# Kernel tuning notes

Measured on AMD Instinct MI355X. Metric: run time of the kernel, lower is better.

## Reference

```python
import jax, jax.numpy as jnp
import numpy as np

N = 50000      # nodes
E = 800000     # edges (before self-loops)
F_IN = 128     # num_features
H = 4          # heads
C = 64         # hidden_channels
HC = H * C     # 256
NEG_SLOPE = 0.2


def setup_inputs() -> dict:
    key = jax.random.key(0)
    ks = jax.random.split(key, 20)
    x = jax.random.normal(ks[0], (N, F_IN), dtype=jnp.float32)
    edge_index = jax.random.randint(ks[1], (2, E), 0, N, dtype=jnp.int32)
    s = 0.05
    inp = {"x": x, "edge_index": edge_index}
    dims_in = [F_IN, HC, HC, HC]
    for l in range(4):
        kW, ka, kb = jax.random.split(ks[2 + l], 3)
        inp[f"W{l+1}"] = jax.random.normal(kW, (dims_in[l], HC), dtype=jnp.float32) * s
        inp[f"a_src{l+1}"] = jax.random.normal(ka, (H, C), dtype=jnp.float32) * s
        inp[f"a_dst{l+1}"] = jax.random.normal(kb, (H, C), dtype=jnp.float32) * s
        inp[f"b{l+1}"] = jnp.zeros((HC,), dtype=jnp.float32)
    return inp


def gat_conv(x, src, dst, W, a_src, a_dst, b):
    # x: [N, F_in] -> h: [N, H, C]
    h = (x @ W).reshape(N, H, C)
    es = jnp.sum(h * a_src, axis=-1)  # [N, H] per-node source logits
    ed = jnp.sum(h * a_dst, axis=-1)  # [N, H]
    e = jax.nn.leaky_relu(es[src] + ed[dst], NEG_SLOPE)  # [Etot, H]
    m = jax.ops.segment_max(e, dst, num_segments=N)      # per-dst max
    m = jnp.where(jnp.isfinite(m), m, 0.0)
    ex = jnp.exp(e - m[dst])
    denom = jax.ops.segment_sum(ex, dst, num_segments=N)
    alpha = ex / (denom[dst] + 1e-16)                     # edge softmax
    out = jax.ops.segment_sum(alpha[:, :, None] * h[src], dst, num_segments=N)
    return out.reshape(N, HC) + b


def reference(x, edge_index,
              W1, a_src1, a_dst1, b1,
              W2, a_src2, a_dst2, b2,
              W3, a_src3, a_dst3, b3,
              W4, a_src4, a_dst4, b4):
    loop = jnp.arange(N, dtype=edge_index.dtype)
    src = jnp.concatenate([edge_index[0], loop])  # add self-loops (PyG default)
    dst = jnp.concatenate([edge_index[1], loop])
    x1 = jax.nn.relu(gat_conv(x, src, dst, W1, a_src1, a_dst1, b1))
    x2 = jax.nn.relu(gat_conv(x1, src, dst, W2, a_src2, a_dst2, b2))
    x3 = jax.nn.relu(gat_conv(x2 + x1, src, dst, W3, a_src3, a_dst3, b3))
    x4 = jax.nn.relu(gat_conv(x2 + x3, src, dst, W4, a_src4, a_dst4, b4))
    # NOTE: source code calls conv4 again (not conv5) -- reproduced faithfully
    x5 = gat_conv(x4 + x3, src, dst, W4, a_src4, a_dst4, b4)
    return x5
```

## Files before the change

### kernel.cpp

```cpp
#include <hip/hip_runtime.h>
#include <hip/hip_bf16.h>

#define N_NODES 50000
#define E_EDGES 800000
#define ETOT (E_EDGES + N_NODES)
#define HC 256
#define NHEAD 4
#define CHAN 64
#define NEG 0.2f
#define NBLK ((N_NODES + 1023) / 1024)

typedef _Float16 half8 __attribute__((ext_vector_type(8)));
typedef _Float16 half4v __attribute__((ext_vector_type(4)));
typedef float float4v __attribute__((ext_vector_type(4)));


__global__ __launch_bounds__(256) void count_rank_kernel(const int* __restrict__ ei,
                                                         int* __restrict__ counts,
                                                         int* __restrict__ rank) {
    int base = blockIdx.x * 1024 + threadIdx.x;
    int dst[4];
    bool val[4];
    #pragma unroll
    for (int r = 0; r < 4; ++r) {
        int i = base + r * 256;
        val[r] = (i < ETOT);
        dst[r] = 0;
        if (val[r]) dst[r] = (i < E_EDGES) ? ei[E_EDGES + i] : (i - E_EDGES);
    }
    int rk[4];
    #pragma unroll
    for (int r = 0; r < 4; ++r)
        if (val[r]) rk[r] = atomicAdd(&counts[dst[r]], 1);
    #pragma unroll
    for (int r = 0; r < 4; ++r)
        if (val[r]) rank[base + r * 256] = rk[r];
}

__global__ __launch_bounds__(256) void blocksum_kernel(const int* __restrict__ counts,
                                                       int* __restrict__ blocksums) {
    __shared__ int s[4];
    int b = blockIdx.x, tid = threadIdx.x;
    int base = b * 1024;
    int sum = 0;
    #pragma unroll
    for (int r = 0; r < 4; ++r) {
        int idx = base + r * 256 + tid;
        sum += (idx < N_NODES) ? counts[idx] : 0;
    }
    #pragma unroll
    for (int m = 1; m < 64; m <<= 1) sum += __shfl_xor(sum, m, 64);
    if ((tid & 63) == 0) s[tid >> 6] = sum;
    __syncthreads();
    if (tid == 0) blocksums[b] = s[0] + s[1] + s[2] + s[3];
}

__global__ __launch_bounds__(64) void blockscan_kernel(int* __restrict__ blocksums) {
    int tid = threadIdx.x;
    int v = (tid < NBLK) ? blocksums[tid] : 0;
    #pragma unroll
    for (int off = 1; off < 64; off <<= 1) {
        int t = __shfl_up(v, off, 64);
        if (tid >= off) v += t;
    }
    if (tid < NBLK) blocksums[tid] = v;
}

__global__ __launch_bounds__(1024) void scatter_scan_kernel(const int* __restrict__ counts,
                                                            const int* __restrict__ blocksums,
                                                            int* __restrict__ offsets) {
    __shared__ int s[1024];
    int b = blockIdx.x, tid = threadIdx.x;
    int idx = b * 1024 + tid;
    int v = (idx < N_NODES) ? counts[idx] : 0;
    s[tid] = v;
    __syncthreads();
    for (int off = 1; off < 1024; off <<= 1) {
        int t = (tid >= off) ? s[tid - off] : 0;
        __syncthreads();
        s[tid] += t;
        __syncthreads();
    }
    int excl = s[tid] - v + (b > 0 ? blocksums[b - 1] : 0);
    if (idx < N_NODES) offsets[idx] = excl;
    if (idx == N_NODES - 1) offsets[N_NODES] = excl + v;
}

__global__ __launch_bounds__(256) void fill_kernel(const int* __restrict__ ei,
                                                   const int* __restrict__ rank,
                                                   const int* __restrict__ offsets,
                                                   int2* __restrict__ csr) {
    int base = blockIdx.x * 1024 + threadIdx.x;
    #pragma unroll
    for (int r = 0; r < 4; ++r) {
        int i = base + r * 256;
        if (i >= ETOT) continue;
        int src, dst;
        if (i < E_EDGES) { src = ei[i]; dst = ei[E_EDGES + i]; }
        else             { src = i - E_EDGES; dst = src; }
        int pos = offsets[dst] + rank[i];
        csr[pos] = make_int2(src, dst);
    }
}


__global__ __launch_bounds__(256) void wsplit_all_kernel(
        const float* __restrict__ W0, const float* __restrict__ W1,
        const float* __restrict__ W2, const float* __restrict__ W3,
        _Float16* __restrict__ Th0, _Float16* __restrict__ Tl0,
        _Float16* __restrict__ Th1, _Float16* __restrict__ Tl1,
        _Float16* __restrict__ Th2, _Float16* __restrict__ Tl2,
        _Float16* __restrict__ Th3, _Float16* __restrict__ Tl3) {
    int id = blockIdx.x * 256 + threadIdx.x;
    const float* W; _Float16 *Th, *Tl; int K;
    if (id < 32768)       { W = W0; Th = Th0; Tl = Tl0; K = 128; }
    else if (id < 98304)  { W = W1; Th = Th1; Tl = Tl1; K = 256; id -= 32768; }
    else if (id < 163840) { W = W2; Th = Th2; Tl = Tl2; K = 256; id -= 98304; }
    else if (id < 229376) { W = W3; Th = Th3; Tl = Tl3; K = 256; id -= 163840; }
    else return;
    int n = id & 255, k = id >> 8;
    float w = W[(size_t)k * 256 + n];
    _Float16 h = (_Float16)w;
    _Float16 l = (_Float16)(w - (float)h);
    Th[(size_t)n * K + k] = h;
    Tl[(size_t)n * K + k] = l;
}

__global__ void xsplit_kernel(const float* __restrict__ x, _Float16* __restrict__ xh,
                              _Float16* __restrict__ xl, int total) {
    int id = blockIdx.x * 256 + threadIdx.x;
    if (id >= total) return;
    float v = x[id];
    _Float16 h = (_Float16)v;
    xh[id] = h;
    xl[id] = (_Float16)(v - (float)h);
}


__global__ __launch_bounds__(256) void edge_alpha_kernel(
        const float* __restrict__ es, const float* __restrict__ ed,
        const int2* __restrict__ csr, _Float16* __restrict__ ex) {
    int e = blockIdx.x * 256 + threadIdx.x;
    if (e >= ETOT) return;
    int2 sd = csr[e];
    float4 esv = *(const float4*)(es + (size_t)sd.x * 4);
    float4 edv = *(const float4*)(ed + (size_t)sd.y * 4);
    float4 v;
    v.x = esv.x + edv.x; v.y = esv.y + edv.y;
    v.z = esv.z + edv.z; v.w = esv.w + edv.w;
    v.x = (v.x > 0.f) ? v.x : NEG * v.x;
    v.y = (v.y > 0.f) ? v.y : NEG * v.y;
    v.z = (v.z > 0.f) ? v.z : NEG * v.z;
    v.w = (v.w > 0.f) ? v.w : NEG * v.w;
    half4v o = {(_Float16)__expf(v.x), (_Float16)__expf(v.y),
                (_Float16)__expf(v.z), (_Float16)__expf(v.w)};
    *(half4v*)(ex + (size_t)e * 4) = o;
}


template<int K, bool HASLO>
struct SmemLayout {
    _Float16 Ah[64][K + 8];
    _Float16 Al[HASLO ? 64 : 1][HASLO ? (K + 8) : 8];
    _Float16 Bh[256][40];
    _Float16 Bl[256][40];
};
template<int K, bool HASLO>
union SmemU {
    SmemLayout<K, HASLO> t;
    _Float16 out[64][264];
};

template<int K, bool HASLO, bool HAS2>
__global__ __launch_bounds__(256) void gemm_mfma_kernel(
        const _Float16* __restrict__ A1h, const _Float16* __restrict__ A1l,
        const _Float16* __restrict__ A2h,
        const _Float16* __restrict__ Wth, const _Float16* __restrict__ Wtl,
        const float* __restrict__ a_src, const float* __restrict__ a_dst,
        _Float16* __restrict__ H16, float* __restrict__ es, float* __restrict__ ed,
        int M) {
    constexpr int NC  = K / 32;
    constexpr int CPR = K / 8;
    __shared__ SmemU<K, HASLO> u;
    auto& Ah = u.t.Ah;
    auto& Al = u.t.Al;
    auto& Bh = u.t.Bh;
    auto& Bl = u.t.Bl;

    int tid = threadIdx.x;
    int m0 = blockIdx.x * 64;
    int w = tid >> 6, lane = tid & 63;
    int rn = w * 64;
    int fr = lane & 15;
    int q  = lane >> 4;
    int fk = q * 8;

    int wr = tid >> 2;
    int wk = (tid & 3) * 8;

    half8 a1c[NC], a2c[HAS2 ? NC : 1], alc[HASLO ? NC : 1];
    #pragma unroll
    for (int c = 0; c < NC; ++c) {
        int idx = c * 256 + tid;
        int row = idx / CPR, col = (idx % CPR) * 8;
        int grow = m0 + row;
        a1c[c] = (half8)(_Float16)0;
        if (grow < M) a1c[c] = *(const half8*)(A1h + (size_t)grow * K + col);
        if constexpr (HAS2) {
            a2c[c] = (half8)(_Float16)0;
            if (grow < M) a2c[c] = *(const half8*)(A2h + (size_t)grow * K + col);
        }
        if constexpr (HASLO) {
            alc[c] = (half8)(_Float16)0;
            if (grow < M) alc[c] = *(const half8*)(A1l + (size_t)grow * K + col);
        }
    }
    half8 pbh[4], pbl[4];
    auto loadB = [&](int k0) {
        #pragma unroll
        for (int g = 0; g < 4; ++g) {
            int r = g * 64 + wr;
            pbh[g] = *(const half8*)(Wth + (size_t)r * K + k0 + wk);
            pbl[g] = *(const half8*)(Wtl + (size_t)r * K + k0 + wk);
        }
    };
    loadB(0);

    #pragma unroll
    for (int c = 0; c < NC; ++c) {
        int idx = c * 256 + tid;
        int row = idx / CPR, col = (idx % CPR) * 8;
        half8 v = a1c[c];
        if constexpr (HAS2) v = v + a2c[c];
        *(half8*)&Ah[row][col] = v;
        if constexpr (HASLO) *(half8*)&Al[row][col] = alc[c];
    }

    float4v acc[4][4];
    #pragma unroll
    for (int i = 0; i < 4; ++i)
        #pragma unroll
        for (int j = 0; j < 4; ++j)
            acc[i][j] = (float4v){0.f, 0.f, 0.f, 0.f};

    __syncthreads();

    for (int kk = 0; kk < K / 32; ++kk) {
        int k0 = kk * 32;
        #pragma unroll
        for (int g = 0; g < 4; ++g) {
            int r = g * 64 + wr;
            *(half8*)&Bh[r][wk] = pbh[g];
            *(half8*)&Bl[r][wk] = pbl[g];
        }
        __syncthreads();
        if (kk + 1 < K / 32) loadB(k0 + 32);
        half8 afh[4], bfh[4], bfl[4];
        #pragma unroll
        for (int t = 0; t < 4; ++t) {
            afh[t] = *(const half8*)&Ah[t * 16 + fr][k0 + fk];
            bfh[t] = *(const half8*)&Bh[rn + t * 16 + fr][fk];
            bfl[t] = *(const half8*)&Bl[rn + t * 16 + fr][fk];
        }
        if constexpr (HASLO) {
            half8 afl[4];
            #pragma unroll
            for (int t = 0; t < 4; ++t) afl[t] = *(const half8*)&Al[t * 16 + fr][k0 + fk];
            #pragma unroll
            for (int tm = 0; tm < 4; ++tm)
                #pragma unroll
                for (int tn = 0; tn < 4; ++tn)
                    acc[tm][tn] = __builtin_amdgcn_mfma_f32_16x16x32_f16(
                        afl[tm], bfh[tn], acc[tm][tn], 0, 0, 0);
        }
        #pragma unroll
        for (int tm = 0; tm < 4; ++tm)
            #pragma unroll
            for (int tn = 0; tn < 4; ++tn) {
                float4v c = acc[tm][tn];
                c = __builtin_amdgcn_mfma_f32_16x16x32_f16(afh[tm], bfl[tn], c, 0, 0, 0);
                c = __builtin_amdgcn_mfma_f32_16x16x32_f16(afh[tm], bfh[tn], c, 0, 0, 0);
                acc[tm][tn] = c;
            }
        __syncthreads();
    }

    float asv[4], adv[4];
    #pragma unroll
    for (int tn = 0; tn < 4; ++tn) {
        asv[tn] = a_src[w * CHAN + tn * 16 + fr];
        adv[tn] = a_dst[w * CHAN + tn * 16 + fr];
    }
    #pragma unroll
    for (int tm = 0; tm < 4; ++tm) {
        #pragma unroll
        for (int i = 0; i < 4; ++i) {
            int r = tm * 16 + q * 4 + i;
            float ps = 0.f, pd = 0.f;
            #pragma unroll
            for (int tn = 0; tn < 4; ++tn) {
                float hv = acc[tm][tn][i];
                ps += hv * asv[tn];
                pd += hv * adv[tn];
                u.out[r][rn + tn * 16 + fr] = (_Float16)hv;
            }
            #pragma unroll
            for (int msk = 1; msk < 16; msk <<= 1) {
                ps += __shfl_xor(ps, msk, 64);
                pd += __shfl_xor(pd, msk, 64);
            }
            int row = m0 + r;
            if (fr == 0 && row < M) {
                es[row * NHEAD + w] = ps;
                ed[row * NHEAD + w] = pd;
            }
        }
    }
    __syncthreads();

    #pragma unroll
    for (int k = 0; k < 8; ++k) {
        int c = k * 256 + tid;
        int r = c >> 5, cc = c & 31;
        if (m0 + r < M) {
            half8 v = *(const half8*)(&u.out[r][0] + cc * 8);
            *(half8*)(H16 + (size_t)(m0 + r) * HC + cc * 8) = v;
        }
    }
}


__global__ __launch_bounds__(256) void gat_aggregate_kernel(
        const _Float16* __restrict__ H16, const _Float16* __restrict__ ex,
        const int* __restrict__ offsets, const int2* __restrict__ csr,
        const float* __restrict__ bias, _Float16* __restrict__ out16,
        float* __restrict__ out32, int do_relu, int node_base) {
    __shared__ float ex_lds[4][256];
    __shared__ int   src_lds[4][64];
    int tid = threadIdx.x;
    int w = tid >> 6, lane = tid & 63;
    int n = node_base + blockIdx.x * 4 + w;
    int off = offsets[n];
    int deg = offsets[n + 1] - off;

    if (deg <= 64) {
        int sreg = n;
        half4v exh = (half4v)(_Float16)0;
        if (lane < deg) {
            sreg = csr[off + lane].x;
            exh = *(const half4v*)(ex + (size_t)(off + lane) * 4);
        }
        float4 ex4 = make_float4((float)exh[0], (float)exh[1], (float)exh[2], (float)exh[3]);
        src_lds[w][lane] = sreg;
        *(float4*)&ex_lds[w][lane * 4] = ex4;

        int hl = lane & 31, side = lane >> 5;
        int hd = hl >> 3;
        float av[8] = {0.f, 0.f, 0.f, 0.f, 0.f, 0.f, 0.f, 0.f};
        int degr = (deg + 7) & ~7;
        #pragma unroll 2
        for (int j0 = 0; j0 < degr; j0 += 8) {
            int j = j0 + side;
            int s0 = src_lds[w][j];
            int s1 = src_lds[w][j + 2];
            int s2 = src_lds[w][j + 4];
            int s3 = src_lds[w][j + 6];
            float w0 = ex_lds[w][j * 4 + hd];
            float w1 = ex_lds[w][(j + 2) * 4 + hd];
            float w2 = ex_lds[w][(j + 4) * 4 + hd];
            float w3 = ex_lds[w][(j + 6) * 4 + hd];
            half8 h0 = *(const half8*)(H16 + (size_t)s0 * HC + hl * 8);
            half8 h1 = *(const half8*)(H16 + (size_t)s1 * HC + hl * 8);
            half8 h2 = *(const half8*)(H16 + (size_t)s2 * HC + hl * 8);
            half8 h3 = *(const half8*)(H16 + (size_t)s3 * HC + hl * 8);
            #pragma unroll
            for (int c = 0; c < 8; ++c) {
                av[c] += w0 * (float)h0[c];
                av[c] += w1 * (float)h1[c];
                av[c] += w2 * (float)h2[c];
                av[c] += w3 * (float)h3[c];
            }
        }

        float4 l4 = ex4;
        #pragma unroll
        for (int msk = 1; msk < 64; msk <<= 1) {
            l4.x += __shfl_xor(l4.x, msk, 64);
            l4.y += __shfl_xor(l4.y, msk, 64);
            l4.z += __shfl_xor(l4.z, msk, 64);
            l4.w += __shfl_xor(l4.w, msk, 64);
        }
        #pragma unroll
        for (int c = 0; c < 8; ++c) av[c] += __shfl_xor(av[c], 32, 64);
        if (side == 0) {
            float denom = (hd == 0) ? l4.x : (hd == 1) ? l4.y : (hd == 2) ? l4.z : l4.w;
            float scale = 1.f / (denom + 1e-16f);
            float4 b0 = *(const float4*)(bias + hl * 8);
            float4 b1 = *(const float4*)(bias + hl * 8 + 4);
            float o[8] = {av[0] * scale + b0.x, av[1] * scale + b0.y,
                          av[2] * scale + b0.z, av[3] * scale + b0.w,
                          av[4] * scale + b1.x, av[5] * scale + b1.y,
                          av[6] * scale + b1.z, av[7] * scale + b1.w};
            if (do_relu)
                #pragma unroll
                for (int c = 0; c < 8; ++c) o[c] = fmaxf(o[c], 0.f);
            if (out16) {
                half8 ov = {(_Float16)o[0], (_Float16)o[1], (_Float16)o[2], (_Float16)o[3],
                            (_Float16)o[4], (_Float16)o[5], (_Float16)o[6], (_Float16)o[7]};
                *(half8*)(out16 + (size_t)n * HC + hl * 8) = ov;
            } else {
                *(float4*)(out32 + (size_t)n * HC + hl * 8) =
                    make_float4(o[0], o[1], o[2], o[3]);
                *(float4*)(out32 + (size_t)n * HC + hl * 8 + 4) =
                    make_float4(o[4], o[5], o[6], o[7]);
            }
        }
        return;
    }

    int head = lane >> 4;
    float4 acc0 = make_float4(0.f, 0.f, 0.f, 0.f);
    float den = 0.f;
    for (int j = 0; j < deg; ++j) {
        int s = csr[off + j].x;
        float exv = (float)ex[(size_t)(off + j) * 4 + head];
        den += exv;
        half4v h0 = *(const half4v*)(H16 + (size_t)s * HC + lane * 4);
        acc0.x += exv * (float)h0[0]; acc0.y += exv * (float)h0[1];
        acc0.z += exv * (float)h0[2]; acc0.w += exv * (float)h0[3];
    }
    float scale = 1.f / (den + 1e-16f);
    float4 b4 = *(const float4*)(bias + lane * 4);
    float o[4] = {acc0.x * scale + b4.x, acc0.y * scale + b4.y,
                  acc0.z * scale + b4.z, acc0.w * scale + b4.w};
    if (do_relu)
        #pragma unroll
        for (int c = 0; c < 4; ++c) o[c] = fmaxf(o[c], 0.f);
    if (out16) {
        half4v ov = {(_Float16)o[0], (_Float16)o[1], (_Float16)o[2], (_Float16)o[3]};
        *(half4v*)(out16 + (size_t)n * HC + lane * 4) = ov;
    } else {
        *(float4*)(out32 + (size_t)n * HC + lane * 4) = make_float4(o[0], o[1], o[2], o[3]);
    }
}


extern "C" void kernel_launch(void* const* d_in, const int* in_sizes, int n_in,
                              void* d_out, int out_size, void* d_ws, size_t ws_size,
                              hipStream_t stream) {
    const float* x  = (const float*)d_in[0];
    const int*   ei = (const int*)d_in[1];
    const float *W[5], *Asrc[5], *Adst[5], *Bs[5];
    for (int l = 0; l < 4; ++l) {
        W[l]    = (const float*)d_in[2 + l * 4];
        Asrc[l] = (const float*)d_in[3 + l * 4];
        Adst[l] = (const float*)d_in[4 + l * 4];
        Bs[l]   = (const float*)d_in[5 + l * 4];
    }
    W[4] = W[3]; Asrc[4] = Asrc[3]; Adst[4] = Adst[3]; Bs[4] = Bs[3];

    char* ws = (char*)d_ws;
    size_t off = 0;
    auto alloc = [&](size_t bytes) -> void* {
        void* p = ws + off;
        off += (bytes + 255) & ~(size_t)255;
        return p;
    };
    _Float16* h16  = (_Float16*)alloc((size_t)N_NODES * HC * 2);
    _Float16* xa   = (_Float16*)alloc((size_t)N_NODES * HC * 2);
    _Float16* xb   = (_Float16*)alloc((size_t)N_NODES * HC * 2);
    _Float16* xc   = (_Float16*)alloc((size_t)N_NODES * HC * 2);
    _Float16* xd   = (_Float16*)alloc((size_t)N_NODES * HC * 2);
    _Float16* xh   = (_Float16*)alloc((size_t)N_NODES * 128 * 2);
    _Float16* xl   = (_Float16*)alloc((size_t)N_NODES * 128 * 2);
    float* es      = (float*)alloc((size_t)N_NODES * 4 * 4);
    float* ed      = (float*)alloc((size_t)N_NODES * 4 * 4);
    _Float16* exbuf = (_Float16*)alloc((size_t)ETOT * 4 * 2);
    int*   counts  = (int*)alloc((size_t)N_NODES * 4);
    int*   offsets = (int*)alloc((size_t)(N_NODES + 1) * 4);
    int*   rank    = (int*)alloc((size_t)ETOT * 4);
    int2*  csr     = (int2*)alloc((size_t)ETOT * 8);
    int*   blocksums = (int*)alloc((size_t)NBLK * 4);
    _Float16 *Wth[5], *Wtl[5];
    int Ks[4] = {128, 256, 256, 256};
    for (int l = 0; l < 4; ++l) {
        Wth[l] = (_Float16*)alloc((size_t)256 * Ks[l] * 2);
        Wtl[l] = (_Float16*)alloc((size_t)256 * Ks[l] * 2);
    }
    Wth[4] = Wth[3]; Wtl[4] = Wtl[3];

    hipMemsetAsync(counts, 0, (size_t)N_NODES * 4, stream);
    count_rank_kernel<<<(ETOT + 1023) / 1024, 256, 0, stream>>>(ei, counts, rank);
    blocksum_kernel<<<NBLK, 256, 0, stream>>>(counts, blocksums);
    blockscan_kernel<<<1, 64, 0, stream>>>(blocksums);
    scatter_scan_kernel<<<NBLK, 1024, 0, stream>>>(counts, blocksums, offsets);
    fill_kernel<<<(ETOT + 1023) / 1024, 256, 0, stream>>>(ei, rank, offsets, csr);
    wsplit_all_kernel<<<(229376 + 255) / 256, 256, 0, stream>>>(
        W[0], W[1], W[2], W[3],
        Wth[0], Wtl[0], Wth[1], Wtl[1], Wth[2], Wtl[2], Wth[3], Wtl[3]);
    xsplit_kernel<<<(N_NODES * 128 + 255) / 256, 256, 0, stream>>>(x, xh, xl, N_NODES * 128);

    int gemm_grid = (N_NODES + 63) / 64;
    auto agg = [&](int l, _Float16* o16, float* o32, int relu) {
        edge_alpha_kernel<<<(ETOT + 255) / 256, 256, 0, stream>>>(
            es, ed, csr, exbuf);
        gat_aggregate_kernel<<<N_NODES / 8, 256, 0, stream>>>(
            h16, exbuf, offsets, csr, Bs[l], o16, o32, relu, 0);
        gat_aggregate_kernel<<<N_NODES / 8, 256, 0, stream>>>(
            h16, exbuf, offsets, csr, Bs[l], o16, o32, relu, N_NODES / 2);
    };

    float* out = (float*)d_out;
    gemm_mfma_kernel<128, true, false><<<gemm_grid, 256, 0, stream>>>(
        xh, xl, nullptr, Wth[0], Wtl[0], Asrc[0], Adst[0], h16, es, ed, N_NODES);
    agg(0, xa, nullptr, 1);
    gemm_mfma_kernel<256, false, false><<<gemm_grid, 256, 0, stream>>>(
        xa, nullptr, nullptr, Wth[1], Wtl[1], Asrc[1], Adst[1], h16, es, ed, N_NODES);
    agg(1, xb, nullptr, 1);
    gemm_mfma_kernel<256, false, true><<<gemm_grid, 256, 0, stream>>>(
        xb, nullptr, xa, Wth[2], Wtl[2], Asrc[2], Adst[2], h16, es, ed, N_NODES);
    agg(2, xc, nullptr, 1);
    gemm_mfma_kernel<256, false, true><<<gemm_grid, 256, 0, stream>>>(
        xb, nullptr, xc, Wth[3], Wtl[3], Asrc[3], Adst[3], h16, es, ed, N_NODES);
    agg(3, xd, nullptr, 1);
    gemm_mfma_kernel<256, false, true><<<gemm_grid, 256, 0, stream>>>(
        xd, nullptr, xc, Wth[4], Wtl[4], Asrc[4], Adst[4], h16, es, ed, N_NODES);
    agg(4, nullptr, out, 0);
}
```

Measured before the change: 743.6 us.

## Load GEMM B fragments directly from global memory, drop LDS staging of weights

The GEMM kernel stops staging weight tiles through shared memory with per-k-step barriers. Each wave now reads its B fragments straight from global/L2 inside the k-loop, with an unroll of two and a single barrier after the loop. This shrinks LDS use, which may allow more blocks per CU, and removes two syncs per k-step, at the cost of redundant, less coalesced global loads of the weights. The two half-graph aggregate launches are also merged into one launch over all nodes.

```diff
diff --git a/kernel.cpp b/kernel.cpp
--- a/kernel.cpp
+++ b/kernel.cpp
@@ -159,15 +159,13 @@
 
 
 template<int K, bool HASLO>
-struct SmemLayout {
+struct SmemA {
     _Float16 Ah[64][K + 8];
     _Float16 Al[HASLO ? 64 : 1][HASLO ? (K + 8) : 8];
-    _Float16 Bh[256][40];
-    _Float16 Bl[256][40];
 };
 template<int K, bool HASLO>
 union SmemU {
-    SmemLayout<K, HASLO> t;
+    SmemA<K, HASLO> t;
     _Float16 out[64][264];
 };
 
@@ -184,8 +182,6 @@
     __shared__ SmemU<K, HASLO> u;
     auto& Ah = u.t.Ah;
     auto& Al = u.t.Al;
-    auto& Bh = u.t.Bh;
-    auto& Bl = u.t.Bl;
 
     int tid = threadIdx.x;
     int m0 = blockIdx.x * 64;
@@ -195,45 +191,33 @@
     int q  = lane >> 4;
     int fk = q * 8;
 
-    int wr = tid >> 2;
-    int wk = (tid & 3) * 8;
-
-    half8 a1c[NC], a2c[HAS2 ? NC : 1], alc[HASLO ? NC : 1];
-    #pragma unroll
-    for (int c = 0; c < NC; ++c) {
-        int idx = c * 256 + tid;
-        int row = idx / CPR, col = (idx % CPR) * 8;
-        int grow = m0 + row;
-        a1c[c] = (half8)(_Float16)0;
-        if (grow < M) a1c[c] = *(const half8*)(A1h + (size_t)grow * K + col);
-        if constexpr (HAS2) {
-            a2c[c] = (half8)(_Float16)0;
-            if (grow < M) a2c[c] = *(const half8*)(A2h + (size_t)grow * K + col);
-        }
-        if constexpr (HASLO) {
-            alc[c] = (half8)(_Float16)0;
-            if (grow < M) alc[c] = *(const half8*)(A1l + (size_t)grow * K + col);
-        }
-    }
-    half8 pbh[4], pbl[4];
-    auto loadB = [&](int k0) {
-        #pragma unroll
-        for (int g = 0; g < 4; ++g) {
-            int r = g * 64 + wr;
-            pbh[g] = *(const half8*)(Wth + (size_t)r * K + k0 + wk);
-            pbl[g] = *(const half8*)(Wtl + (size_t)r * K + k0 + wk);
-        }
-    };
-    loadB(0);
-
-    #pragma unroll
-    for (int c = 0; c < NC; ++c) {
-        int idx = c * 256 + tid;
-        int row = idx / CPR, col = (idx % CPR) * 8;
-        half8 v = a1c[c];
-        if constexpr (HAS2) v = v + a2c[c];
-        *(half8*)&Ah[row][col] = v;
-        if constexpr (HASLO) *(half8*)&Al[row][col] = alc[c];
+    {
+        half8 a1c[NC], a2c[HAS2 ? NC : 1], alc[HASLO ? NC : 1];
+        #pragma unroll
+        for (int c = 0; c < NC; ++c) {
+            int idx = c * 256 + tid;
+            int row = idx / CPR, col = (idx % CPR) * 8;
+            int grow = m0 + row;
+            a1c[c] = (half8)(_Float16)0;
+            if (grow < M) a1c[c] = *(const half8*)(A1h + (size_t)grow * K + col);
+            if constexpr (HAS2) {
+                a2c[c] = (half8)(_Float16)0;
+                if (grow < M) a2c[c] = *(const half8*)(A2h + (size_t)grow * K + col);
+            }
+            if constexpr (HASLO) {
+                alc[c] = (half8)(_Float16)0;
+                if (grow < M) alc[c] = *(const half8*)(A1l + (size_t)grow * K + col);
+            }
+        }
+        #pragma unroll
+        for (int c = 0; c < NC; ++c) {
+            int idx = c * 256 + tid;
+            int row = idx / CPR, col = (idx % CPR) * 8;
+            half8 v = a1c[c];
+            if constexpr (HAS2) v = v + a2c[c];
+            *(half8*)&Ah[row][col] = v;
+            if constexpr (HASLO) *(half8*)&Al[row][col] = alc[c];
+        }
     }
 
     float4v acc[4][4];
@@ -245,45 +229,33 @@
 
     __syncthreads();
 
+    const _Float16* bh_base = Wth + (size_t)(rn + fr) * K + fk;
+    const _Float16* bl_base = Wtl + (size_t)(rn + fr) * K + fk;
+    #pragma unroll 2
     for (int kk = 0; kk < K / 32; ++kk) {
         int k0 = kk * 32;
-        #pragma unroll
-        for (int g = 0; g < 4; ++g) {
-            int r = g * 64 + wr;
-            *(half8*)&Bh[r][wk] = pbh[g];
-            *(half8*)&Bl[r][wk] = pbl[g];
-        }
-        __syncthreads();
-        if (kk + 1 < K / 32) loadB(k0 + 32);
-        half8 afh[4], bfh[4], bfl[4];
+        half8 afh[4], afl[4];
         #pragma unroll
         for (int t = 0; t < 4; ++t) {
             afh[t] = *(const half8*)&Ah[t * 16 + fr][k0 + fk];
-            bfh[t] = *(const half8*)&Bh[rn + t * 16 + fr][fk];
-            bfl[t] = *(const half8*)&Bl[rn + t * 16 + fr][fk];
-        }
-        if constexpr (HASLO) {
-            half8 afl[4];
+            if constexpr (HASLO) afl[t] = *(const half8*)&Al[t * 16 + fr][k0 + fk];
+        }
+        #pragma unroll
+        for (int tn = 0; tn < 4; ++tn) {
+            half8 bh = *(const half8*)(bh_base + (size_t)tn * 16 * K + k0);
+            half8 bl = *(const half8*)(bl_base + (size_t)tn * 16 * K + k0);
             #pragma unroll
-            for (int t = 0; t < 4; ++t) afl[t] = *(const half8*)&Al[t * 16 + fr][k0 + fk];
-            #pragma unroll
-            for (int tm = 0; tm < 4; ++tm)
-                #pragma unroll
-                for (int tn = 0; tn < 4; ++tn)
-                    acc[tm][tn] = __builtin_amdgcn_mfma_f32_16x16x32_f16(
-                        afl[tm], bfh[tn], acc[tm][tn], 0, 0, 0);
-        }
-        #pragma unroll
-        for (int tm = 0; tm < 4; ++tm)
-            #pragma unroll
-            for (int tn = 0; tn < 4; ++tn) {
+            for (int tm = 0; tm < 4; ++tm) {
                 float4v c = acc[tm][tn];
-                c = __builtin_amdgcn_mfma_f32_16x16x32_f16(afh[tm], bfl[tn], c, 0, 0, 0);
-                c = __builtin_amdgcn_mfma_f32_16x16x32_f16(afh[tm], bfh[tn], c, 0, 0, 0);
+                if constexpr (HASLO)
+                    c = __builtin_amdgcn_mfma_f32_16x16x32_f16(afl[tm], bh, c, 0, 0, 0);
+                c = __builtin_amdgcn_mfma_f32_16x16x32_f16(afh[tm], bl, c, 0, 0, 0);
+                c = __builtin_amdgcn_mfma_f32_16x16x32_f16(afh[tm], bh, c, 0, 0, 0);
                 acc[tm][tn] = c;
             }
-        __syncthreads();
-    }
+        }
+    }
+    __syncthreads();
 
     float asv[4], adv[4];
     #pragma unroll
@@ -334,12 +306,12 @@
         const _Float16* __restrict__ H16, const _Float16* __restrict__ ex,
         const int* __restrict__ offsets, const int2* __restrict__ csr,
         const float* __restrict__ bias, _Float16* __restrict__ out16,
-        float* __restrict__ out32, int do_relu, int node_base) {
+        float* __restrict__ out32, int do_relu) {
     __shared__ float ex_lds[4][256];
     __shared__ int   src_lds[4][64];
     int tid = threadIdx.x;
     int w = tid >> 6, lane = tid & 63;
-    int n = node_base + blockIdx.x * 4 + w;
+    int n = blockIdx.x * 4 + w;
     int off = offsets[n];
     int deg = offsets[n + 1] - off;
 
@@ -504,10 +476,8 @@
     auto agg = [&](int l, _Float16* o16, float* o32, int relu) {
         edge_alpha_kernel<<<(ETOT + 255) / 256, 256, 0, stream>>>(
             es, ed, csr, exbuf);
-        gat_aggregate_kernel<<<N_NODES / 8, 256, 0, stream>>>(
-            h16, exbuf, offsets, csr, Bs[l], o16, o32, relu, 0);
-        gat_aggregate_kernel<<<N_NODES / 8, 256, 0, stream>>>(
-            h16, exbuf, offsets, csr, Bs[l], o16, o32, relu, N_NODES / 2);
+        gat_aggregate_kernel<<<N_NODES / 4, 256, 0, stream>>>(
+            h16, exbuf, offsets, csr, Bs[l], o16, o32, relu);
     };
 
     float* out = (float*)d_out;
```

Result: slower. 766.4 us (+3.1%).
